# Optimization experiments

Measured on AMD Instinct MI355X. Metric: run time of the kernel, lower is better.

The kernel has to match this reference:

```python
import jax, jax.numpy as jnp
import numpy as np

N_NODES = 50000
N_EDGES = 1600000
D_IN = 128
D_HID = 128


def setup_inputs() -> dict:
    key = jax.random.key(0)
    ks = jax.random.split(key, 6)
    edge_index = jax.random.randint(ks[0], (2, N_EDGES), 0, N_NODES, dtype=jnp.int32)
    emb = jax.random.normal(ks[1], (N_NODES, D_IN), dtype=jnp.float32) * 0.1
    W1 = jax.random.normal(ks[2], (D_IN, D_HID), dtype=jnp.float32) * (1.0 / np.sqrt(D_IN))
    b1 = jnp.zeros((D_HID,), dtype=jnp.float32)
    W2 = jax.random.normal(ks[3], (D_HID, D_HID), dtype=jnp.float32) * (1.0 / np.sqrt(D_HID))
    b2 = jnp.zeros((D_HID,), dtype=jnp.float32)
    head_w = jax.random.normal(ks[4], (D_HID, 1), dtype=jnp.float32) * (1.0 / np.sqrt(D_HID))
    head_b = jnp.zeros((1,), dtype=jnp.float32)
    return {"edge_index": edge_index, "emb": emb, "W1": W1, "b1": b1,
            "W2": W2, "b2": b2, "head_w": head_w, "head_b": head_b}


def _gcn_norm(edge_index, num_nodes):
    # PyG GCNConv default: add self-loops, sym-normalize D^-1/2 (A+I) D^-1/2.
    loops = jnp.arange(num_nodes, dtype=edge_index.dtype)
    src = jnp.concatenate([edge_index[0], loops])  # [E+N]
    dst = jnp.concatenate([edge_index[1], loops])  # [E+N]
    deg = jax.ops.segment_sum(jnp.ones_like(dst, dtype=jnp.float32), dst,
                              num_segments=num_nodes)  # [N], >=1 via self-loops
    dis = jax.lax.rsqrt(deg)
    norm = dis[src] * dis[dst]  # [E+N]
    return src, dst, norm


def _gcn_conv(x, W, b, src, dst, norm, num_nodes):
    h = x @ W                                  # [N, D] dense transform first
    msg = h[src] * norm[:, None]               # [E+N, D] gather + scale
    out = jax.ops.segment_sum(msg, dst, num_segments=num_nodes)  # scatter-add
    return out + b


def reference(edge_index, emb, W1, b1, W2, b2, head_w, head_b):
    src, dst, norm = _gcn_norm(edge_index, N_NODES)
    x = jax.nn.relu(_gcn_conv(emb, W1, b1, src, dst, norm, N_NODES))
    x = jax.nn.relu(_gcn_conv(x, W2, b2, src, dst, norm, N_NODES))
    scores = jax.nn.sigmoid(x @ head_w + head_b)[:, 0]  # [N]
    return scores
```

## Files before the change

kernel.cpp:

```cpp
#include <hip/hip_runtime.h>
#include <hip/hip_fp16.h>
#include <math.h>

#define D 128
#define D4 32
#define AP 136
#define AP8 144
#define NBUCK 256
#define EPB 8192
#define BCAP2 8192

typedef _Float16 f16x8 __attribute__((ext_vector_type(8)));
typedef float f32x4 __attribute__((ext_vector_type(4)));
typedef float f32x2 __attribute__((ext_vector_type(2)));


__global__ void prep_all_kernel(const float* __restrict__ W1, _Float16* __restrict__ Wt1,
                                const float* __restrict__ W2, _Float16* __restrict__ Wt2,
                                int* __restrict__ bcnt) {
    int t = threadIdx.x;
    if (blockIdx.x == 0) bcnt[t] = 0;
    int half = blockIdx.x & 63;
    const float* W = (blockIdx.x < 64) ? W1 : W2;
    _Float16* Wt   = (blockIdx.x < 64) ? Wt1 : Wt2;
    int i = half * 256 + t;
    int k = i >> 7, c = i & 127;
    Wt[c * 128 + k] = (_Float16)W[i];
}


__global__ __launch_bounds__(256) void bucket_pass1(const int* __restrict__ src,
                                                    const int* __restrict__ dst,
                                                    int* __restrict__ bcnt,
                                                    unsigned* __restrict__ buckets,
                                                    int E, unsigned magicM) {
    __shared__ unsigned stage[EPB];
    __shared__ int lcnt[NBUCK], loff[NBUCK], gbase[NBUCK];

    int t = threadIdx.x;
    int base = blockIdx.x * EPB;
    int nblk = min(EPB, E - base);
    lcnt[t] = 0;
    __syncthreads();

    for (int i = t; i < nblk; i += 256) {
        unsigned d = (unsigned)dst[base + i];
        int b = (int)(((unsigned long long)d * magicM) >> 24);
        atomicAdd(&lcnt[b], 1);
    }
    __syncthreads();

    int v = lcnt[t];
    loff[t] = v;
    __syncthreads();
    for (int off = 1; off < 256; off <<= 1) {
        int x = (t >= off) ? loff[t - off] : 0;
        __syncthreads();
        loff[t] += x;
        __syncthreads();
    }
    int incl = loff[t];
    __syncthreads();
    loff[t] = incl - v;
    gbase[t] = atomicAdd(&bcnt[t], v);
    lcnt[t] = 0;
    __syncthreads();

    for (int i = t; i < nblk; i += 256) {
        unsigned s = (unsigned)src[base + i];
        unsigned d = (unsigned)dst[base + i];
        unsigned pk = (s << 16) | d;
        int b = (int)(((unsigned long long)d * magicM) >> 24);
        int p = atomicAdd(&lcnt[b], 1);
        stage[loff[b] + p] = pk;
    }
    __syncthreads();

    for (int i = t; i < nblk; i += 256) {
        unsigned pk = stage[i];
        int b = (int)(((unsigned long long)(pk & 0xffffu) * magicM) >> 24);
        int pos = gbase[b] + (i - loff[b]);
        if (pos < BCAP2) buckets[(size_t)b * BCAP2 + pos] = pk;
    }
}

__global__ __launch_bounds__(256) void csr_pass2(const unsigned* __restrict__ buckets,
                                                 const int* __restrict__ bcnt,
                                                 int* __restrict__ row_ptr,
                                                 float* __restrict__ dis,
                                                 unsigned short* __restrict__ col,
                                                 int N, int npb, int E) {
    __shared__ int cnt[256], sc[256], excl[256];
    __shared__ unsigned short estage[16384];

    int b = blockIdx.x;
    int t = threadIdx.x;

    int bv = min(bcnt[t], BCAP2);
    sc[t] = bv;
    __syncthreads();
    for (int off = 1; off < 256; off <<= 1) {
        int x = (t >= off) ? sc[t - off] : 0;
        __syncthreads();
        sc[t] += x;
        __syncthreads();
    }
    int base = sc[b] - min(bcnt[b], BCAP2);
    if (b == 0 && t == 0) row_ptr[N] = E;
    __syncthreads();

    int lo = b * npb;
    int nn = min(npb, N - lo);
    int n = min(bcnt[b], BCAP2);
    const unsigned* bk = buckets + (size_t)b * BCAP2;

    cnt[t] = 0;
    __syncthreads();
    for (int i = t; i < n; i += 256) {
        int dl = (int)(bk[i] & 0xffffu) - lo;
        atomicAdd(&cnt[dl], 1);
    }
    __syncthreads();
    int v = cnt[t];
    sc[t] = v;
    __syncthreads();
    for (int off = 1; off < 256; off <<= 1) {
        int x = (t >= off) ? sc[t - off] : 0;
        __syncthreads();
        sc[t] += x;
        __syncthreads();
    }
    excl[t] = sc[t] - v;
    if (t < nn) {
        row_ptr[lo + t] = base + excl[t];
        dis[lo + t] = rsqrtf((float)v + 1.0f);
    }
    cnt[t] = 0;
    __syncthreads();
    for (int i = t; i < n; i += 256) {
        unsigned pk = bk[i];
        int dl = (int)(pk & 0xffffu) - lo;
        int p = atomicAdd(&cnt[dl], 1);
        estage[excl[dl] + p] = (unsigned short)(pk >> 16);
    }
    __syncthreads();
    for (int i = t; i < n; i += 256) col[base + i] = estage[i];
}


#define GEMM_CORE                                                            \
    const uint4* Wt16 = (const uint4*)Wt;                                    \
    for (int i = t; i < 128 * 16; i += 256) {                                \
        int r = i >> 4, ch = i & 15;                                         \
        *(uint4*)&Ws[r * AP + ch * 8] = Wt16[i];                             \
    }                                                                        \
    __syncthreads();                                                         \
    int wave = t >> 6;                                                       \
    int lane = t & 63;                                                       \
    int m16 = lane & 15;                                                     \
    int quad = lane >> 4;                                                    \
    f32x4 acc[8];                                                            \
    for (int n = 0; n < 8; n++) acc[n] = (f32x4){0.f, 0.f, 0.f, 0.f};        \
    _Pragma("unroll")                                                        \
    for (int kc = 0; kc < 4; kc++) {                                         \
        f16x8 a = *(const f16x8*)&As[(wave * 16 + m16) * AP + kc * 32 + quad * 8]; \
        _Pragma("unroll")                                                    \
        for (int n = 0; n < 8; n++) {                                        \
            f16x8 bfrag = *(const f16x8*)&Ws[(n * 16 + m16) * AP + kc * 32 + quad * 8]; \
            acc[n] = __builtin_amdgcn_mfma_f32_16x16x32_f16(a, bfrag, acc[n], 0, 0, 0); \
        }                                                                    \
    }                                                                        \
    __syncthreads();                                                         \
    unsigned char* Cs8 = (unsigned char*)As;                                 \
    float dv[4];                                                             \
    _Pragma("unroll")                                                        \
    for (int r = 0; r < 4; r++) {                                            \
        int grow = row0 + wave * 16 + quad * 4 + r;                          \
        dv[r] = (grow < N) ? dis[grow] : 0.f;                                \
    }                                                                        \
    _Pragma("unroll")                                                        \
    for (int n = 0; n < 8; n++)                                              \
        _Pragma("unroll")                                                    \
        for (int r = 0; r < 4; r++) {                                        \
            float val = acc[n][r] * dv[r];                                   \
            int wq = __builtin_amdgcn_cvt_pk_fp8_f32(val, val, 0, false);    \
            Cs8[(wave * 16 + quad * 4 + r) * AP8 + n * 16 + m16] = (unsigned char)(wq & 0xff); \
        }                                                                    \
    __syncthreads();                                                         \
    uint4* C16 = (uint4*)C8;                                                 \
    for (int i = lane; i < 128; i += 64) {                                   \
        int r = i >> 3, ch = i & 7;                                          \
        int grow = row0 + wave * 16 + r;                                     \
        if (grow < N)                                                        \
            C16[(size_t)grow * 8 + ch] = *(const uint4*)&Cs8[(wave * 16 + r) * AP8 + ch * 16]; \
    }

__global__ __launch_bounds__(256) void gemm_f32a_fp8c(const float* __restrict__ A,
                                                      const _Float16* __restrict__ Wt,
                                                      const float* __restrict__ dis,
                                                      unsigned int* __restrict__ C8, int N) {
    __shared__ _Float16 As[64 * AP];
    __shared__ _Float16 Ws[128 * AP];
    int t = threadIdx.x;
    int row0 = blockIdx.x * 64;
    const float4* A4 = (const float4*)A;
    for (int i = t; i < 64 * 16; i += 256) {
        int r = i >> 4, ch = i & 15;
        uint4 v = make_uint4(0, 0, 0, 0);
        if (row0 + r < N) {
            float4 a0 = A4[(size_t)(row0 + r) * 32 + ch * 2];
            float4 a1 = A4[(size_t)(row0 + r) * 32 + ch * 2 + 1];
            __half2 h0 = __floats2half2_rn(a0.x, a0.y);
            __half2 h1 = __floats2half2_rn(a0.z, a0.w);
            __half2 h2 = __floats2half2_rn(a1.x, a1.y);
            __half2 h3 = __floats2half2_rn(a1.z, a1.w);
            v.x = *(unsigned*)&h0; v.y = *(unsigned*)&h1;
            v.z = *(unsigned*)&h2; v.w = *(unsigned*)&h3;
        }
        *(uint4*)&As[r * AP + ch * 8] = v;
    }
    GEMM_CORE
}

__global__ __launch_bounds__(256) void gemm_f16a_fp8c(const _Float16* __restrict__ A,
                                                      const _Float16* __restrict__ Wt,
                                                      const float* __restrict__ dis,
                                                      unsigned int* __restrict__ C8, int N) {
    __shared__ _Float16 As[64 * AP];
    __shared__ _Float16 Ws[128 * AP];
    int t = threadIdx.x;
    int row0 = blockIdx.x * 64;
    const uint4* A16 = (const uint4*)A;
    for (int i = t; i < 64 * 16; i += 256) {
        int r = i >> 4, ch = i & 15;
        uint4 v = make_uint4(0, 0, 0, 0);
        if (row0 + r < N) v = A16[(size_t)(row0 + r) * 16 + ch];
        *(uint4*)&As[r * AP + ch * 8] = v;
    }
    GEMM_CORE
}


__device__ __forceinline__ void acc8(float4& a, unsigned int u) {
    f32x2 lo = __builtin_amdgcn_cvt_pk_f32_fp8((int)u, false);
    f32x2 hi = __builtin_amdgcn_cvt_pk_f32_fp8((int)u, true);
    a.x += lo[0]; a.y += lo[1]; a.z += hi[0]; a.w += hi[1];
}

#define AGG8_BODY                                                               \
    float4 acc = make_float4(0.f, 0.f, 0.f, 0.f);                               \
    acc8(acc, t8[(size_t)node * D4 + lane]);        \
    int e0 = row_ptr[node], e1 = row_ptr[node + 1];                             \
    int deg = e1 - e0;                                                          \
    for (int base = 0; base < deg; base += 32) {                                \
        int cnt = min(32, deg - base);                                          \
        int myc = (base + lane < deg) ? (int)col[e0 + base + lane] : 0;         \
        int j = 0;                                                              \
        for (; j + 8 <= cnt; j += 8) {                                          \
            int s0 = __shfl(myc, j + 0, 32); int s1 = __shfl(myc, j + 1, 32);   \
            int s2 = __shfl(myc, j + 2, 32); int s3 = __shfl(myc, j + 3, 32);   \
            int s4 = __shfl(myc, j + 4, 32); int s5 = __shfl(myc, j + 5, 32);   \
            int s6 = __shfl(myc, j + 6, 32); int s7 = __shfl(myc, j + 7, 32);   \
            unsigned int u0 = t8[(size_t)s0 * D4 + lane];                       \
            unsigned int u1 = t8[(size_t)s1 * D4 + lane];                       \
            unsigned int u2 = t8[(size_t)s2 * D4 + lane];                       \
            unsigned int u3 = t8[(size_t)s3 * D4 + lane];                       \
            unsigned int u4 = t8[(size_t)s4 * D4 + lane];                       \
            unsigned int u5 = t8[(size_t)s5 * D4 + lane];                       \
            unsigned int u6 = t8[(size_t)s6 * D4 + lane];                       \
            unsigned int u7 = t8[(size_t)s7 * D4 + lane];                       \
            acc8(acc, u0); acc8(acc, u1); acc8(acc, u2); acc8(acc, u3);         \
            acc8(acc, u4); acc8(acc, u5); acc8(acc, u6); acc8(acc, u7);         \
        }                                                                       \
        for (; j < cnt; j++) {                                                  \
            int s = __shfl(myc, j, 32);                                         \
            acc8(acc, t8[(size_t)s * D4 + lane]);                               \
        }                                                                       \
    }                                                                           \
    float di = dis[node];                                                       \
    float4 bb = ((const float4*)bias)[lane];                                    \
    float4 o;                                                                   \
    o.x = fmaxf(fmaf(di, acc.x, bb.x), 0.f);                                    \
    o.y = fmaxf(fmaf(di, acc.y, bb.y), 0.f);                                    \
    o.z = fmaxf(fmaf(di, acc.z, bb.z), 0.f);                                    \
    o.w = fmaxf(fmaf(di, acc.w, bb.w), 0.f);

__global__ void agg_fp8_kernel(const unsigned int* __restrict__ t8, const float* __restrict__ bias,
                               const int* __restrict__ row_ptr, const unsigned short* __restrict__ col,
                               const float* __restrict__ dis, _Float16* __restrict__ xout, int N) {
    int t = threadIdx.x;
    int node = blockIdx.x * 8 + (t >> 5);
    int lane = t & 31;
    if (node >= N) return;
    AGG8_BODY
    __half2 q0 = __floats2half2_rn(o.x, o.y);
    __half2 q1 = __floats2half2_rn(o.z, o.w);
    uint2 u;
    u.x = *(unsigned int*)&q0;
    u.y = *(unsigned int*)&q1;
    ((uint2*)xout)[(size_t)node * D4 + lane] = u;
}

__global__ void agg_head_fp8_kernel(const unsigned int* __restrict__ t8, const float* __restrict__ bias,
                                    const int* __restrict__ row_ptr, const unsigned short* __restrict__ col,
                                    const float* __restrict__ dis,
                                    const float* __restrict__ head_w, const float* __restrict__ head_b,
                                    float* __restrict__ out, int N) {
    int t = threadIdx.x;
    int node = blockIdx.x * 8 + (t >> 5);
    int lane = t & 31;
    if (node >= N) return;
    AGG8_BODY
    float4 wv = ((const float4*)head_w)[lane];
    float s = o.x * wv.x + o.y * wv.y + o.z * wv.z + o.w * wv.w;
    for (int m = 1; m < 32; m <<= 1) s += __shfl_xor(s, m, 64);
    if (lane == 0) {
        float v = s + head_b[0];
        out[node] = 1.0f / (1.0f + expf(-v));
    }
}


extern "C" void kernel_launch(void* const* d_in, const int* in_sizes, int n_in,
                              void* d_out, int out_size, void* d_ws, size_t ws_size,
                              hipStream_t stream) {
    const int*   edge   = (const int*)d_in[0];
    const float* emb    = (const float*)d_in[1];
    const float* W1     = (const float*)d_in[2];
    const float* b1     = (const float*)d_in[3];
    const float* W2     = (const float*)d_in[4];
    const float* b2     = (const float*)d_in[5];
    const float* head_w = (const float*)d_in[6];
    const float* head_b = (const float*)d_in[7];
    float* out = (float*)d_out;

    int E = in_sizes[0] / 2;
    int N = in_sizes[1] / D;
    const int* srcp = edge;
    const int* dstp = edge + E;

    char* w = (char*)d_ws;
    auto alloc = [&](size_t bytes) -> char* {
        char* p = w;
        w += (bytes + 15) & ~(size_t)15;
        return p;
    };
    unsigned int*   t8      = (unsigned int*)alloc((size_t)N * D);
    _Float16*       x1h     = (_Float16*)alloc((size_t)N * D * 2);
    unsigned*       buckets = (unsigned*)alloc((size_t)NBUCK * BCAP2 * 4);
    _Float16*       Wt1     = (_Float16*)alloc((size_t)D * D * 2);
    _Float16*       Wt2     = (_Float16*)alloc((size_t)D * D * 2);
    unsigned short* col     = (unsigned short*)alloc((size_t)E * 2);
    int*            bcnt    = (int*)alloc(NBUCK * 4);
    int*            row_ptr = (int*)alloc((size_t)(N + 1) * 4);
    float*          dis     = (float*)alloc((size_t)N * 4);

    int npb = (N + NBUCK - 1) / NBUCK;
    unsigned magicM = (16777216u + (unsigned)npb - 1) / (unsigned)npb;
    int gP1 = (E + EPB - 1) / EPB;
    int gG = (N + 63) / 64;
    int gA = (N + 7) / 8;

    prep_all_kernel<<<128, 256, 0, stream>>>(W1, Wt1, W2, Wt2, bcnt);
    bucket_pass1<<<gP1, 256, 0, stream>>>(srcp, dstp, bcnt, buckets, E, magicM);
    csr_pass2<<<NBUCK, 256, 0, stream>>>(buckets, bcnt, row_ptr, dis, col, N, npb, E);

    gemm_f32a_fp8c<<<gG, 256, 0, stream>>>(emb, Wt1, dis, t8, N);
    agg_fp8_kernel<<<gA, 256, 0, stream>>>(t8, b1, row_ptr, col, dis, x1h, N);
    gemm_f16a_fp8c<<<gG, 256, 0, stream>>>(x1h, Wt2, dis, t8, N);
    agg_head_fp8_kernel<<<gA, 256, 0, stream>>>(t8, b2, row_ptr, col, dis,
                                                head_w, head_b, out, N);
}
```

Before: 208.6 us.

## Fuse CSR pass2 with first GEMM and layer-1 aggregation with second GEMM

Node degrees are now counted with global atomics in bucket_pass1, so the first GEMM can compute its normalisation directly and run in the same launch as CSR construction, as extra blocks. The layer-1 aggregation is fused into the second GEMM: each block aggregates 64 nodes straight into shared memory and multiplies there, which removes the fp16 x1 intermediate and one launch. EPB is halved, giving more pass1 blocks. The cost is global atomic contention on deg, plus lower aggregation parallelism per block inside the fused kernel.

```diff
diff --git a/kernel.cpp b/kernel.cpp
--- a/kernel.cpp
+++ b/kernel.cpp
@@ -7,18 +7,25 @@
 #define AP 136
 #define AP8 144
 #define NBUCK 256
-#define EPB 8192
+#define EPB 4096
 #define BCAP2 8192
 
 typedef _Float16 f16x8 __attribute__((ext_vector_type(8)));
 typedef float f32x4 __attribute__((ext_vector_type(4)));
 typedef float f32x2 __attribute__((ext_vector_type(2)));
 
+#define SMEM_BYTES 52224
+
 
 __global__ void prep_all_kernel(const float* __restrict__ W1, _Float16* __restrict__ Wt1,
                                 const float* __restrict__ W2, _Float16* __restrict__ Wt2,
-                                int* __restrict__ bcnt) {
-    int t = threadIdx.x;
+                                int* __restrict__ bcnt, int* __restrict__ deg, int N) {
+    int t = threadIdx.x;
+    if (blockIdx.x >= 128) {
+        int i = (blockIdx.x - 128) * 256 + t;
+        if (i < N) deg[i] = 0;
+        return;
+    }
     if (blockIdx.x == 0) bcnt[t] = 0;
     int half = blockIdx.x & 63;
     const float* W = (blockIdx.x < 64) ? W1 : W2;
@@ -33,6 +40,7 @@
                                                     const int* __restrict__ dst,
                                                     int* __restrict__ bcnt,
                                                     unsigned* __restrict__ buckets,
+                                                    int* __restrict__ deg,
                                                     int E, unsigned magicM) {
     __shared__ unsigned stage[EPB];
     __shared__ int lcnt[NBUCK], loff[NBUCK], gbase[NBUCK];
@@ -47,6 +55,7 @@
         unsigned d = (unsigned)dst[base + i];
         int b = (int)(((unsigned long long)d * magicM) >> 24);
         atomicAdd(&lcnt[b], 1);
+        atomicAdd(&deg[d], 1);
     }
     __syncthreads();
 
@@ -84,71 +93,9 @@
     }
 }
 
-__global__ __launch_bounds__(256) void csr_pass2(const unsigned* __restrict__ buckets,
-                                                 const int* __restrict__ bcnt,
-                                                 int* __restrict__ row_ptr,
-                                                 float* __restrict__ dis,
-                                                 unsigned short* __restrict__ col,
-                                                 int N, int npb, int E) {
-    __shared__ int cnt[256], sc[256], excl[256];
-    __shared__ unsigned short estage[16384];
-
-    int b = blockIdx.x;
-    int t = threadIdx.x;
-
-    int bv = min(bcnt[t], BCAP2);
-    sc[t] = bv;
-    __syncthreads();
-    for (int off = 1; off < 256; off <<= 1) {
-        int x = (t >= off) ? sc[t - off] : 0;
-        __syncthreads();
-        sc[t] += x;
-        __syncthreads();
-    }
-    int base = sc[b] - min(bcnt[b], BCAP2);
-    if (b == 0 && t == 0) row_ptr[N] = E;
-    __syncthreads();
-
-    int lo = b * npb;
-    int nn = min(npb, N - lo);
-    int n = min(bcnt[b], BCAP2);
-    const unsigned* bk = buckets + (size_t)b * BCAP2;
-
-    cnt[t] = 0;
-    __syncthreads();
-    for (int i = t; i < n; i += 256) {
-        int dl = (int)(bk[i] & 0xffffu) - lo;
-        atomicAdd(&cnt[dl], 1);
-    }
-    __syncthreads();
-    int v = cnt[t];
-    sc[t] = v;
-    __syncthreads();
-    for (int off = 1; off < 256; off <<= 1) {
-        int x = (t >= off) ? sc[t - off] : 0;
-        __syncthreads();
-        sc[t] += x;
-        __syncthreads();
-    }
-    excl[t] = sc[t] - v;
-    if (t < nn) {
-        row_ptr[lo + t] = base + excl[t];
-        dis[lo + t] = rsqrtf((float)v + 1.0f);
-    }
-    cnt[t] = 0;
-    __syncthreads();
-    for (int i = t; i < n; i += 256) {
-        unsigned pk = bk[i];
-        int dl = (int)(pk & 0xffffu) - lo;
-        int p = atomicAdd(&cnt[dl], 1);
-        estage[excl[dl] + p] = (unsigned short)(pk >> 16);
-    }
-    __syncthreads();
-    for (int i = t; i < n; i += 256) col[base + i] = estage[i];
-}
-
-
-#define GEMM_CORE                                                            \
+
+#define GEMM_CORE(DVEXPR, COUT)                                              \
+    {                                                                        \
     const uint4* Wt16 = (const uint4*)Wt;                                    \
     for (int i = t; i < 128 * 16; i += 256) {                                \
         int r = i >> 4, ch = i & 15;                                         \
@@ -176,7 +123,7 @@
     _Pragma("unroll")                                                        \
     for (int r = 0; r < 4; r++) {                                            \
         int grow = row0 + wave * 16 + quad * 4 + r;                          \
-        dv[r] = (grow < N) ? dis[grow] : 0.f;                                \
+        dv[r] = (grow < N) ? (DVEXPR) : 0.f;                                 \
     }                                                                        \
     _Pragma("unroll")                                                        \
     for (int n = 0; n < 8; n++)                                              \
@@ -187,57 +134,102 @@
             Cs8[(wave * 16 + quad * 4 + r) * AP8 + n * 16 + m16] = (unsigned char)(wq & 0xff); \
         }                                                                    \
     __syncthreads();                                                         \
-    uint4* C16 = (uint4*)C8;                                                 \
-    for (int i = lane; i < 128; i += 64) {                                   \
-        int r = i >> 3, ch = i & 7;                                          \
+    uint4* C16 = (uint4*)(COUT);                                             \
+    for (int i2 = lane; i2 < 128; i2 += 64) {                                \
+        int r = i2 >> 3, ch = i2 & 7;                                        \
         int grow = row0 + wave * 16 + r;                                     \
         if (grow < N)                                                        \
             C16[(size_t)grow * 8 + ch] = *(const uint4*)&Cs8[(wave * 16 + r) * AP8 + ch * 16]; \
-    }
-
-__global__ __launch_bounds__(256) void gemm_f32a_fp8c(const float* __restrict__ A,
-                                                      const _Float16* __restrict__ Wt,
-                                                      const float* __restrict__ dis,
-                                                      unsigned int* __restrict__ C8, int N) {
-    __shared__ _Float16 As[64 * AP];
-    __shared__ _Float16 Ws[128 * AP];
-    int t = threadIdx.x;
-    int row0 = blockIdx.x * 64;
-    const float4* A4 = (const float4*)A;
-    for (int i = t; i < 64 * 16; i += 256) {
-        int r = i >> 4, ch = i & 15;
-        uint4 v = make_uint4(0, 0, 0, 0);
-        if (row0 + r < N) {
-            float4 a0 = A4[(size_t)(row0 + r) * 32 + ch * 2];
-            float4 a1 = A4[(size_t)(row0 + r) * 32 + ch * 2 + 1];
-            __half2 h0 = __floats2half2_rn(a0.x, a0.y);
-            __half2 h1 = __floats2half2_rn(a0.z, a0.w);
-            __half2 h2 = __floats2half2_rn(a1.x, a1.y);
-            __half2 h3 = __floats2half2_rn(a1.z, a1.w);
-            v.x = *(unsigned*)&h0; v.y = *(unsigned*)&h1;
-            v.z = *(unsigned*)&h2; v.w = *(unsigned*)&h3;
+    }                                                                        \
+    }
+
+
+__global__ __launch_bounds__(256) void pass2_gemm1(const unsigned* __restrict__ buckets,
+                                                   const int* __restrict__ bcnt,
+                                                   int* __restrict__ row_ptr,
+                                                   float* __restrict__ dis,
+                                                   unsigned short* __restrict__ col,
+                                                   const float* __restrict__ A,
+                                                   const _Float16* __restrict__ Wt,
+                                                   const int* __restrict__ deg,
+                                                   unsigned int* __restrict__ C8,
+                                                   int N, int npb, int E) {
+    __shared__ __align__(16) char smem[SMEM_BYTES];
+    int t = threadIdx.x;
+
+    if (blockIdx.x >= NBUCK) {
+        _Float16* As = (_Float16*)smem;
+        _Float16* Ws = (_Float16*)(smem + 64 * AP * 2);
+        int row0 = (blockIdx.x - NBUCK) * 64;
+        const float4* A4 = (const float4*)A;
+        for (int i = t; i < 64 * 16; i += 256) {
+            int r = i >> 4, ch = i & 15;
+            uint4 v = make_uint4(0, 0, 0, 0);
+            if (row0 + r < N) {
+                float4 a0 = A4[(size_t)(row0 + r) * 32 + ch * 2];
+                float4 a1 = A4[(size_t)(row0 + r) * 32 + ch * 2 + 1];
+                __half2 h0 = __floats2half2_rn(a0.x, a0.y);
+                __half2 h1 = __floats2half2_rn(a0.z, a0.w);
+                __half2 h2 = __floats2half2_rn(a1.x, a1.y);
+                __half2 h3 = __floats2half2_rn(a1.z, a1.w);
+                v.x = *(unsigned*)&h0; v.y = *(unsigned*)&h1;
+                v.z = *(unsigned*)&h2; v.w = *(unsigned*)&h3;
+            }
+            *(uint4*)&As[r * AP + ch * 8] = v;
         }
-        *(uint4*)&As[r * AP + ch * 8] = v;
-    }
-    GEMM_CORE
-}
-
-__global__ __launch_bounds__(256) void gemm_f16a_fp8c(const _Float16* __restrict__ A,
-                                                      const _Float16* __restrict__ Wt,
-                                                      const float* __restrict__ dis,
-                                                      unsigned int* __restrict__ C8, int N) {
-    __shared__ _Float16 As[64 * AP];
-    __shared__ _Float16 Ws[128 * AP];
-    int t = threadIdx.x;
-    int row0 = blockIdx.x * 64;
-    const uint4* A16 = (const uint4*)A;
-    for (int i = t; i < 64 * 16; i += 256) {
-        int r = i >> 4, ch = i & 15;
-        uint4 v = make_uint4(0, 0, 0, 0);
-        if (row0 + r < N) v = A16[(size_t)(row0 + r) * 16 + ch];
-        *(uint4*)&As[r * AP + ch * 8] = v;
-    }
-    GEMM_CORE
+        GEMM_CORE(rsqrtf((float)deg[grow] + 1.0f), C8)
+        return;
+    }
+
+    int* cnt  = (int*)smem;
+    int* sc   = (int*)(smem + 1024);
+    int* excl = (int*)(smem + 2048);
+    unsigned short* estage = (unsigned short*)(smem + 3072);
+
+    int b = blockIdx.x;
+    int bv = min(bcnt[t], BCAP2);
+    sc[t] = bv;
+    __syncthreads();
+    for (int off = 1; off < 256; off <<= 1) {
+        int x = (t >= off) ? sc[t - off] : 0;
+        __syncthreads();
+        sc[t] += x;
+        __syncthreads();
+    }
+    int base = sc[b] - min(bcnt[b], BCAP2);
+    if (b == 0 && t == 0) row_ptr[N] = E;
+    __syncthreads();
+
+    int lo = b * npb;
+    int nn = min(npb, N - lo);
+    int n = min(bcnt[b], BCAP2);
+    const unsigned* bk = buckets + (size_t)b * BCAP2;
+
+    int vv = (t < nn) ? deg[lo + t] : 0;
+    sc[t] = vv;
+    __syncthreads();
+    for (int off = 1; off < 256; off <<= 1) {
+        int x = (t >= off) ? sc[t - off] : 0;
+        __syncthreads();
+        sc[t] += x;
+        __syncthreads();
+    }
+    excl[t] = sc[t] - vv;
+    if (t < nn) {
+        row_ptr[lo + t] = base + excl[t];
+        dis[lo + t] = rsqrtf((float)vv + 1.0f);
+    }
+    cnt[t] = 0;
+    __syncthreads();
+    for (int i = t; i < n; i += 256) {
+        unsigned pk = bk[i];
+        int dl = (int)(pk & 0xffffu) - lo;
+        int p = atomicAdd(&cnt[dl], 1);
+        int idx = excl[dl] + p;
+        if (idx < BCAP2) estage[idx] = (unsigned short)(pk >> 16);
+    }
+    __syncthreads();
+    for (int i = t; i < n; i += 256) col[base + i] = estage[i];
 }
 
 
@@ -285,21 +277,38 @@
     o.z = fmaxf(fmaf(di, acc.z, bb.z), 0.f);                                    \
     o.w = fmaxf(fmaf(di, acc.w, bb.w), 0.f);
 
-__global__ void agg_fp8_kernel(const unsigned int* __restrict__ t8, const float* __restrict__ bias,
-                               const int* __restrict__ row_ptr, const unsigned short* __restrict__ col,
-                               const float* __restrict__ dis, _Float16* __restrict__ xout, int N) {
-    int t = threadIdx.x;
-    int node = blockIdx.x * 8 + (t >> 5);
-    int lane = t & 31;
-    if (node >= N) return;
-    AGG8_BODY
-    __half2 q0 = __floats2half2_rn(o.x, o.y);
-    __half2 q1 = __floats2half2_rn(o.z, o.w);
-    uint2 u;
-    u.x = *(unsigned int*)&q0;
-    u.y = *(unsigned int*)&q1;
-    ((uint2*)xout)[(size_t)node * D4 + lane] = u;
-}
+
+__global__ __launch_bounds__(256) void agg1_gemm2(const unsigned int* __restrict__ t8,
+                                                  const float* __restrict__ bias,
+                                                  const int* __restrict__ row_ptr,
+                                                  const unsigned short* __restrict__ col,
+                                                  const float* __restrict__ dis,
+                                                  const _Float16* __restrict__ Wt,
+                                                  unsigned int* __restrict__ C8, int N) {
+    __shared__ __align__(16) char smem[SMEM_BYTES];
+    _Float16* As = (_Float16*)smem;
+    _Float16* Ws = (_Float16*)(smem + 64 * AP * 2);
+    int t = threadIdx.x;
+    int row0 = blockIdx.x * 64;
+    {
+        int lane = t & 31;
+        for (int it = 0; it < 8; ++it) {
+            int ln = it * 8 + (t >> 5);
+            int node = row0 + ln;
+            uint2 uo = make_uint2(0u, 0u);
+            if (node < N) {
+                AGG8_BODY
+                __half2 q0 = __floats2half2_rn(o.x, o.y);
+                __half2 q1 = __floats2half2_rn(o.z, o.w);
+                uo.x = *(unsigned int*)&q0;
+                uo.y = *(unsigned int*)&q1;
+            }
+            *(uint2*)&As[ln * AP + lane * 4] = uo;
+        }
+    }
+    GEMM_CORE(dis[grow], C8)
+}
+
 
 __global__ void agg_head_fp8_kernel(const unsigned int* __restrict__ t8, const float* __restrict__ bias,
                                     const int* __restrict__ row_ptr, const unsigned short* __restrict__ col,
@@ -345,8 +354,8 @@
         w += (bytes + 15) & ~(size_t)15;
         return p;
     };
-    unsigned int*   t8      = (unsigned int*)alloc((size_t)N * D);
-    _Float16*       x1h     = (_Float16*)alloc((size_t)N * D * 2);
+    unsigned int*   t8a     = (unsigned int*)alloc((size_t)N * D);
+    unsigned int*   t8b     = (unsigned int*)alloc((size_t)N * D);
     unsigned*       buckets = (unsigned*)alloc((size_t)NBUCK * BCAP2 * 4);
     _Float16*       Wt1     = (_Float16*)alloc((size_t)D * D * 2);
     _Float16*       Wt2     = (_Float16*)alloc((size_t)D * D * 2);
@@ -354,20 +363,20 @@
     int*            bcnt    = (int*)alloc(NBUCK * 4);
     int*            row_ptr = (int*)alloc((size_t)(N + 1) * 4);
     float*          dis     = (float*)alloc((size_t)N * 4);
+    int*            deg     = (int*)alloc((size_t)N * 4);
 
     int npb = (N + NBUCK - 1) / NBUCK;
     unsigned magicM = (16777216u + (unsigned)npb - 1) / (unsigned)npb;
     int gP1 = (E + EPB - 1) / EPB;
     int gG = (N + 63) / 64;
     int gA = (N + 7) / 8;
-
-    prep_all_kernel<<<128, 256, 0, stream>>>(W1, Wt1, W2, Wt2, bcnt);
-    bucket_pass1<<<gP1, 256, 0, stream>>>(srcp, dstp, bcnt, buckets, E, magicM);
-    csr_pass2<<<NBUCK, 256, 0, stream>>>(buckets, bcnt, row_ptr, dis, col, N, npb, E);
-
-    gemm_f32a_fp8c<<<gG, 256, 0, stream>>>(emb, Wt1, dis, t8, N);
-    agg_fp8_kernel<<<gA, 256, 0, stream>>>(t8, b1, row_ptr, col, dis, x1h, N);
-    gemm_f16a_fp8c<<<gG, 256, 0, stream>>>(x1h, Wt2, dis, t8, N);
-    agg_head_fp8_kernel<<<gA, 256, 0, stream>>>(t8, b2, row_ptr, col, dis,
+    int gZ = (N + 255) / 256;
+
+    prep_all_kernel<<<128 + gZ, 256, 0, stream>>>(W1, Wt1, W2, Wt2, bcnt, deg, N);
+    bucket_pass1<<<gP1, 256, 0, stream>>>(srcp, dstp, bcnt, buckets, deg, E, magicM);
+    pass2_gemm1<<<NBUCK + gG, 256, 0, stream>>>(buckets, bcnt, row_ptr, dis, col,
+                                                emb, Wt1, deg, t8a, N, npb, E);
+    agg1_gemm2<<<gG, 256, 0, stream>>>(t8a, b1, row_ptr, col, dis, Wt2, t8b, N);
+    agg_head_fp8_kernel<<<gA, 256, 0, stream>>>(t8b, b2, row_ptr, col, dis,
                                                 head_w, head_b, out, N);
 }
```

New measurement: 293.0 us. +40.5%, slower.
